# Performance work log

Measured on AMD Instinct MI355X. Metric: run time of the kernel, lower is better.

## Reference

```python
import jax, jax.numpy as jnp
import numpy as np

HIDDEN = 1024
HEADS = 16
HEAD_DIM = HIDDEN // HEADS
SCALE = float(np.sqrt(HEAD_DIM))


def setup_inputs() -> dict:
    key = jax.random.key(0)
    ks = jax.random.split(key, 5)
    x = jax.random.normal(ks[0], (2, 2048, HIDDEN), dtype=jnp.float32)
    # qkv_proj: Linear(hidden, 3*hidden); torch stores weight as [out, in]
    w_qkv = jax.random.normal(ks[1], (3 * HIDDEN, HIDDEN), dtype=jnp.float32) / np.sqrt(HIDDEN)
    b_qkv = jax.random.normal(ks[2], (3 * HIDDEN,), dtype=jnp.float32) * 0.02
    w_out = jax.random.normal(ks[3], (HIDDEN, HIDDEN), dtype=jnp.float32) / np.sqrt(HIDDEN)
    b_out = jax.random.normal(ks[4], (HIDDEN,), dtype=jnp.float32) * 0.02
    return {"x": x, "w_qkv": w_qkv, "b_qkv": b_qkv, "w_out": w_out, "b_out": b_out}


def reference(x, w_qkv, b_qkv, w_out, b_out):
    B, S, H = x.shape
    # fused QKV projection -> [B, S, 3, heads, head_dim]
    qkv = (jnp.einsum('bsh,oh->bso', x, w_qkv) + b_qkv).reshape(B, S, 3, HEADS, HEAD_DIM)
    q, k, v = qkv[:, :, 0], qkv[:, :, 1], qkv[:, :, 2]
    scores = jnp.einsum('bqhd,bkhd->bhqk', q, k) / SCALE
    attn = jax.nn.softmax(scores, axis=-1)  # dropout p=0.0 (eval)
    ctx = jnp.einsum('bhqk,bkhd->bqhd', attn, v).reshape(B, S, H)
    return jnp.einsum('bsh,oh->bso', ctx, w_out) + b_out
```

## Files before the change

### kernel.cpp

```cpp
#include <hip/hip_runtime.h>
#include <math.h>

#define BATCH 2
#define SEQ   2048
#define HIDDEN 1024
#define HEADS 16
#define HD    64
#define QSCALE 0.18033688011112042f

typedef __attribute__((ext_vector_type(8)))  short short8;
typedef __attribute__((ext_vector_type(16))) float f32x16;

__device__ __forceinline__ unsigned short f2bf(float f) {
    unsigned int u = __builtin_bit_cast(unsigned int, f);
    u = (u + 0x7FFFu + ((u >> 16) & 1u)) >> 16;
    return (unsigned short)u;
}
__device__ __forceinline__ float bf2f(unsigned short h) {
    unsigned int u = ((unsigned int)h) << 16;
    return __builtin_bit_cast(float, u);
}
__device__ __forceinline__ unsigned int cvt_pk_bf16(float lo, float hi) {
    unsigned int r;
    asm("v_cvt_pk_bf16_f32 %0, %1, %2" : "=v"(r) : "v"(lo), "v"(hi));
    return r;
}
__device__ __forceinline__ void gl16(const void* g, void* l) {
    __builtin_amdgcn_global_load_lds(
        (const __attribute__((address_space(1))) void*)g,
        (__attribute__((address_space(3))) void*)l,
        16, 0, 0);
}
#define WAIT_VM(N) asm volatile("s_waitcnt vmcnt(" #N ")" ::: "memory")
#define BARRIER()  do { __builtin_amdgcn_s_barrier(); __builtin_amdgcn_sched_barrier(0); } while (0)

__global__ __launch_bounds__(256)
void conv_hi(const float* __restrict__ src, unsigned short* __restrict__ hi)
{
    int idx = blockIdx.x * 256 + threadIdx.x;
    float4 v = ((const float4*)src)[idx];
    ushort4 h4;
    h4.x = f2bf(v.x); h4.y = f2bf(v.y); h4.z = f2bf(v.z); h4.w = f2bf(v.w);
    ((ushort4*)hi)[idx] = h4;
}

__device__ __forceinline__ void gemm_core1(
    const char* Ah, const char* Bh,
    int m0, int n0, char* smem, f32x16 acc[2][2])
{
    const int t    = threadIdx.x;
    const int lane = t & 63;
    const int w    = t >> 6;
    const int wm   = w >> 1, wn = w & 1;
    const int l31  = lane & 31, hh = lane >> 5;

    auto stage = [&](int buf, int kt) {
        #pragma unroll
        for (int i = 0; i < 2; ++i) {
            int r  = i * 64 + (t >> 2);
            int cs = (t & 3) ^ ((r >> 1) & 3);
            gl16(Ah + ((size_t)(m0 + r) * 1024 + kt * 32 + cs * 8) * 2,
                 smem + buf * 16384 + i * 4096 + w * 1024);
            gl16(Bh + ((size_t)(n0 + r) * 1024 + kt * 32 + cs * 8) * 2,
                 smem + buf * 16384 + 8192 + i * 4096 + w * 1024);
        }
    };

    stage(0, 0);
    int cur = 0, nxt = 1;
    for (int kt = 0; kt < 32; ++kt) {
        if (kt + 1 < 32) {
            stage(nxt, kt + 1);
            WAIT_VM(4);
        } else {
            WAIT_VM(0);
        }
        BARRIER();
        const char* Ab = smem + cur * 16384;
        const char* Bb = Ab + 8192;
        #pragma unroll
        for (int ks = 0; ks < 2; ++ks) {
            short8 ah[2], bh[2];
            #pragma unroll
            for (int mt = 0; mt < 2; ++mt) {
                int R  = wm * 64 + mt * 32 + l31;
                int ch = ((ks * 2 + hh) ^ ((R >> 1) & 3)) * 16;
                ah[mt] = *(const short8*)(Ab + R * 64 + ch);
            }
            #pragma unroll
            for (int nt = 0; nt < 2; ++nt) {
                int R  = wn * 64 + nt * 32 + l31;
                int ch = ((ks * 2 + hh) ^ ((R >> 1) & 3)) * 16;
                bh[nt] = *(const short8*)(Bb + R * 64 + ch);
            }
            #pragma unroll
            for (int mt = 0; mt < 2; ++mt)
                #pragma unroll
                for (int nt = 0; nt < 2; ++nt)
                    acc[mt][nt] = __builtin_amdgcn_mfma_f32_32x32x16_bf16(ah[mt], bh[nt], acc[mt][nt], 0, 0, 0);
        }
        cur = nxt;
        nxt = (nxt == 2) ? 0 : nxt + 1;
    }
    __syncthreads();
}

__global__ __launch_bounds__(256, 3)
void qkv_gemm(const unsigned short* __restrict__ xh,
              const unsigned short* __restrict__ wh,
              const float* __restrict__ bias,
              unsigned short* __restrict__ qB, unsigned short* __restrict__ kB,
              unsigned short* __restrict__ vtB)
{
    __shared__ __align__(16) char smem[49152];
    f32x16 acc[2][2] = {{{}, {}}, {{}, {}}};
    const int m0 = blockIdx.x * 128, n0 = blockIdx.y * 128;
    gemm_core1((const char*)xh, (const char*)wh, m0, n0, smem, acc);

    const int t    = threadIdx.x;
    const int lane = t & 63;
    const int w    = t >> 6;
    const int wm   = w >> 1, wn = w & 1;
    const int l31  = lane & 31, hh = lane >> 5;

    const int which = n0 >> 10;
    const float scl = (which == 0) ? QSCALE : 1.0f;

    #pragma unroll
    for (int mt = 0; mt < 2; ++mt)
        #pragma unroll
        for (int nt = 0; nt < 2; ++nt) {
            int nl = wn * 64 + nt * 32 + l31;
            float bb = bias[n0 + nl];
            #pragma unroll
            for (int r = 0; r < 16; ++r) {
                int ml = wm * 64 + mt * 32 + (r & 3) + 8 * (r >> 2) + 4 * hh;
                float val = (acc[mt][nt][r] + bb) * scl;
                *(unsigned short*)(smem + ml * 272 + nl * 2) = f2bf(val);
            }
        }
    __syncthreads();

    const int hbase = (n0 & 1023) >> 6;
    const int b     = m0 >> 11;
    const int s0    = m0 & 2047;

    if (which < 2) {
        unsigned short* pp = which ? kB : qB;
        const int nc   = t & 31;
        const int head = hbase + (nc >> 4);
        const int d0   = (nc & 15) * 4;
        #pragma unroll
        for (int it = 0; it < 16; ++it) {
            int m = it * 8 + (t >> 5);
            ushort4 h4 = *(const ushort4*)(smem + m * 272 + nc * 8);
            size_t idx = (((size_t)(b * HEADS + head)) * SEQ + s0 + m) * HD + d0;
            *(ushort4*)&pp[idx] = h4;
        }
    } else {
        const int nl   = t & 127;
        const int head = hbase + (nl >> 6);
        const int d    = nl & 63;
        #pragma unroll
        for (int it = 0; it < 16; ++it) {
            int mq = it * 2 + (t >> 7);
            ushort4 h4;
            h4.x = *(const unsigned short*)(smem + (mq * 4 + 0) * 272 + nl * 2);
            h4.y = *(const unsigned short*)(smem + (mq * 4 + 1) * 272 + nl * 2);
            h4.z = *(const unsigned short*)(smem + (mq * 4 + 2) * 272 + nl * 2);
            h4.w = *(const unsigned short*)(smem + (mq * 4 + 3) * 272 + nl * 2);
            size_t idx = (((size_t)(b * HEADS + head)) * HD + d) * SEQ + s0 + mq * 4;
            *(ushort4*)&vtB[idx] = h4;
        }
    }
}

__global__ __launch_bounds__(256, 3)
void out_gemm(const unsigned short* __restrict__ cth,
              const unsigned short* __restrict__ bh_,
              const float* __restrict__ bias, float* __restrict__ out)
{
    __shared__ __align__(16) char smem[49152];
    f32x16 acc[2][2] = {{{}, {}}, {{}, {}}};
    const int m0 = blockIdx.x * 128, n0 = blockIdx.y * 128;
    gemm_core1((const char*)cth, (const char*)bh_, m0, n0, smem, acc);

    const int t    = threadIdx.x;
    const int lane = t & 63;
    const int w    = t >> 6;
    const int wm   = w >> 1, wn = w & 1;
    const int l31  = lane & 31, hh = lane >> 5;

    #pragma unroll
    for (int mt = 0; mt < 2; ++mt)
        #pragma unroll
        for (int nt = 0; nt < 2; ++nt) {
            int n = n0 + wn * 64 + nt * 32 + l31;
            float bb = bias[n];
            #pragma unroll
            for (int r = 0; r < 16; ++r) {
                int m = m0 + wm * 64 + mt * 32 + (r & 3) + 8 * (r >> 2) + 4 * hh;
                out[(size_t)m * 1024 + n] = acc[mt][nt][r] + bb;
            }
        }
}

#define NPAIR (SEQ / 64)

__global__ __launch_bounds__(256, 2)
void attn_mfma(const unsigned short* __restrict__ qB, const unsigned short* __restrict__ kB,
               const unsigned short* __restrict__ vtB, unsigned short* __restrict__ ctxb)
{
    __shared__ __align__(16) char smem[65536];
    const int t    = threadIdx.x;
    const int lane = t & 63;
    const int wq   = t >> 6;
    const int l31  = lane & 31;
    const int hh   = lane >> 5;

    const int bid = blockIdx.x;
    const int xcd = bid & 7, j = bid >> 3;
    const int qt  = j & 15;
    const int bhg = xcd + 8 * (j >> 4);
    const int q0  = qt * 128;
    const size_t bh = (size_t)bhg;

    const char* qP = (const char*)(qB + bh * SEQ * HD);
    const char* kP = (const char*)(kB + bh * SEQ * HD);
    const char* vP = (const char*)(vtB + bh * SEQ * HD);

    const int wbase = wq * 1024;

    {
        int rr = t >> 3, cc = t & 7;
        #pragma unroll
        for (int i = 0; i < 4; ++i) {
            int row = i * 32 + rr;
            int ch  = cc ^ (row & 7);
            gl16(qP + (size_t)(q0 + row) * 128 + ch * 16, smem + i * 4096 + wbase);
        }
    }
    auto stagePair = [&](int p) {
        int base = ((p + 1) & 3) * 16384;
        int rr = t >> 3;
        int ch = (t & 7) ^ (rr & 7);
        gl16(kP + (size_t)(p * 64 + rr) * 128 + ch * 16,      smem + base +     0 + wbase);
        gl16(kP + (size_t)(p * 64 + 32 + rr) * 128 + ch * 16, smem + base +  4096 + wbase);
        int rr2 = t >> 2;
        int s4  = (rr2 & 3) ^ ((rr2 >> 2) & 3);
        int ch2 = (t & 3) ^ s4;
        gl16(vP + (size_t)rr2 * (SEQ * 2) + p * 128 +      ch2 * 16, smem + base +  8192 + wbase);
        gl16(vP + (size_t)rr2 * (SEQ * 2) + p * 128 + 64 + ch2 * 16, smem + base + 12288 + wbase);
    };
    stagePair(0);
    stagePair(1);
    WAIT_VM(8);
    BARRIER();

    short8 qf[4];
    {
        int qrow = 32 * wq + l31;
        #pragma unroll
        for (int ks = 0; ks < 4; ++ks) {
            int ch = ((2 * ks + hh) ^ (qrow & 7)) * 16;
            qf[ks] = *(const short8*)(smem + qrow * 128 + ch);
        }
    }
    asm volatile("s_waitcnt lgkmcnt(0)" ::: "memory");
    __builtin_amdgcn_sched_barrier(0);

    f32x16 acc0 = {}, acc1 = {};
    float lsum = 0.0f;

    for (int i = 0; i < NPAIR; ++i) {
        if (i + 2 < NPAIR) { stagePair(i + 2); WAIT_VM(8); }
        else if (i + 1 < NPAIR) { WAIT_VM(4); }
        else { WAIT_VM(0); }
        BARRIER();

        const char* Pb = smem + ((i + 1) & 3) * 16384;

        f32x16 sa = {}, sb = {};
        __builtin_amdgcn_s_setprio(1);
        #pragma unroll
        for (int ks = 0; ks < 4; ++ks) {
            int ch = ((2 * ks + hh) ^ (l31 & 7)) * 16;
            short8 ka = *(const short8*)(Pb +        l31 * 128 + ch);
            short8 kb = *(const short8*)(Pb + 4096 + l31 * 128 + ch);
            sa = __builtin_amdgcn_mfma_f32_32x32x16_bf16(ka, qf[ks], sa, 0, 0, 0);
            sb = __builtin_amdgcn_mfma_f32_32x32x16_bf16(kb, qf[ks], sb, 0, 0, 0);
        }
        __builtin_amdgcn_s_setprio(0);

        unsigned int pa_[8], pb_[8];
        float ps0 = 0.f, ps1 = 0.f, ps2 = 0.f, ps3 = 0.f;
        #pragma unroll
        for (int w = 0; w < 8; ++w) {
            float e0 = __builtin_amdgcn_exp2f(sa[2 * w]);
            float e1 = __builtin_amdgcn_exp2f(sa[2 * w + 1]);
            ps0 += e0; ps1 += e1;
            pa_[w] = cvt_pk_bf16(e0, e1);
            float f0 = __builtin_amdgcn_exp2f(sb[2 * w]);
            float f1 = __builtin_amdgcn_exp2f(sb[2 * w + 1]);
            ps2 += f0; ps3 += f1;
            pb_[w] = cvt_pk_bf16(f0, f1);
        }
        lsum += (ps0 + ps1) + (ps2 + ps3);

        const char* Va = Pb + 8192;
        const char* Vb = Pb + 12288;
        __builtin_amdgcn_s_setprio(1);
        #pragma unroll
        for (int ks = 0; ks < 2; ++ks) {
            unsigned int a0 = pa_[4*ks],     a2 = pa_[4*ks + 2];
            unsigned int a1 = pa_[4*ks + 1], a3 = pa_[4*ks + 3];
            asm volatile("v_permlane32_swap_b32 %0, %1" : "+v"(a0), "+v"(a2));
            asm volatile("v_permlane32_swap_b32 %0, %1" : "+v"(a1), "+v"(a3));
            unsigned int b0 = pb_[4*ks],     b2 = pb_[4*ks + 2];
            unsigned int b1 = pb_[4*ks + 1], b3 = pb_[4*ks + 3];
            asm volatile("v_permlane32_swap_b32 %0, %1" : "+v"(b0), "+v"(b2));
            asm volatile("v_permlane32_swap_b32 %0, %1" : "+v"(b1), "+v"(b3));
            short8 pA = __builtin_bit_cast(short8, make_uint4(a0, a1, a2, a3));
            short8 pB = __builtin_bit_cast(short8, make_uint4(b0, b1, b2, b3));
            #pragma unroll
            for (int mt = 0; mt < 2; ++mt) {
                int rrow = 32 * mt + l31;
                int s4   = (rrow & 3) ^ ((rrow >> 2) & 3);
                int ch   = ((2 * ks + hh) ^ s4) * 16;
                short8 va = *(const short8*)(Va + rrow * 64 + ch);
                short8 vb = *(const short8*)(Vb + rrow * 64 + ch);
                if (mt == 0) {
                    acc0 = __builtin_amdgcn_mfma_f32_32x32x16_bf16(va, pA, acc0, 0, 0, 0);
                    acc0 = __builtin_amdgcn_mfma_f32_32x32x16_bf16(vb, pB, acc0, 0, 0, 0);
                } else {
                    acc1 = __builtin_amdgcn_mfma_f32_32x32x16_bf16(va, pA, acc1, 0, 0, 0);
                    acc1 = __builtin_amdgcn_mfma_f32_32x32x16_bf16(vb, pB, acc1, 0, 0, 0);
                }
            }
        }
        __builtin_amdgcn_s_setprio(0);
    }

    lsum += __shfl_xor(lsum, 32, 64);
    __syncthreads();
    float inv = 1.0f / lsum;
    {
        int q = 32 * wq + l31;
        #pragma unroll
        for (int mt = 0; mt < 2; ++mt) {
            #pragma unroll
            for (int m2 = 0; m2 < 4; ++m2) {
                ushort4 h4;
                if (mt == 0) {
                    h4.x = f2bf(acc0[4*m2+0] * inv); h4.y = f2bf(acc0[4*m2+1] * inv);
                    h4.z = f2bf(acc0[4*m2+2] * inv); h4.w = f2bf(acc0[4*m2+3] * inv);
                } else {
                    h4.x = f2bf(acc1[4*m2+0] * inv); h4.y = f2bf(acc1[4*m2+1] * inv);
                    h4.z = f2bf(acc1[4*m2+2] * inv); h4.w = f2bf(acc1[4*m2+3] * inv);
                }
                int d0 = 4 * hh + 8 * m2 + 32 * mt;
                int c  = (d0 >> 3) ^ (q & 7);
                *(ushort4*)(smem + q * 128 + c * 16 + (d0 & 7) * 2) = h4;
            }
        }
    }
    __syncthreads();
    {
        #pragma unroll
        for (int it = 0; it < 4; ++it) {
            int slot = it * 256 + t;
            int row  = slot >> 3;
            int p    = slot & 7;
            uint4 v4 = *(const uint4*)(smem + row * 128 + ((p ^ (row & 7)) * 16));
            *(uint4*)&ctxb[((size_t)(bhg >> 4) * SEQ + q0 + row) * HIDDEN
                           + (bhg & 15) * HD + p * 8] = v4;
        }
    }
}

extern "C" void kernel_launch(void* const* d_in, const int* in_sizes, int n_in,
                              void* d_out, int out_size, void* d_ws, size_t ws_size,
                              hipStream_t stream)
{
    const float* x     = (const float*)d_in[0];
    const float* w_qkv = (const float*)d_in[1];
    const float* b_qkv = (const float*)d_in[2];
    const float* w_out = (const float*)d_in[3];
    const float* b_out = (const float*)d_in[4];
    float* out = (float*)d_out;

    const size_t PH = (size_t)BATCH * HEADS * SEQ * HD;
    unsigned short* ws = (unsigned short*)d_ws;
    unsigned short* qB  = ws;
    unsigned short* kB  = ws + PH;
    unsigned short* vtB = ws + 2 * PH;
    unsigned short* wqh = ws + 3 * PH;
    unsigned short* woh = wqh + 3 * PH / 4;
    unsigned short* cth = woh + PH / 4;
    unsigned short* xh  = (unsigned short*)d_out;

    conv_hi<<<4096, 256, 0, stream>>>(x, xh);
    conv_hi<<<3072, 256, 0, stream>>>(w_qkv, wqh);
    conv_hi<<<1024, 256, 0, stream>>>(w_out, woh);
    qkv_gemm<<<dim3(32, 24), 256, 0, stream>>>(xh, wqh, b_qkv, qB, kB, vtB);
    attn_mfma<<<512, 256, 0, stream>>>(qB, kB, vtB, cth);
    out_gemm<<<dim3(32, 8), 256, 0, stream>>>(cth, woh, b_out, out);
}
```

Before: 114.0 us.

## Software-pipeline QK^T one tile ahead in attention and merge conversion launches

The attention loop now computes the QK^T scores for the next K/V pair before doing the exp and PV work for the current pair. This lets MFMA score work overlap with the softmax exponentials and the V matmul. The vmcnt waits are loosened to match. Separately, the three fp32-to-bf16 conversion launches are merged into one kernel that picks its source from the block index, saving launch overhead. The trade-off is more live registers from the extra score accumulators, which could lower occupancy, and more complex wait-count logic that has to stay correct.

```diff
diff --git a/kernel.cpp b/kernel.cpp
--- a/kernel.cpp
+++ b/kernel.cpp
@@ -16,10 +16,6 @@
     u = (u + 0x7FFFu + ((u >> 16) & 1u)) >> 16;
     return (unsigned short)u;
 }
-__device__ __forceinline__ float bf2f(unsigned short h) {
-    unsigned int u = ((unsigned int)h) << 16;
-    return __builtin_bit_cast(float, u);
-}
 __device__ __forceinline__ unsigned int cvt_pk_bf16(float lo, float hi) {
     unsigned int r;
     asm("v_cvt_pk_bf16_f32 %0, %1, %2" : "=v"(r) : "v"(lo), "v"(hi));
@@ -35,13 +31,22 @@
 #define BARRIER()  do { __builtin_amdgcn_s_barrier(); __builtin_amdgcn_sched_barrier(0); } while (0)
 
 __global__ __launch_bounds__(256)
-void conv_hi(const float* __restrict__ src, unsigned short* __restrict__ hi)
-{
-    int idx = blockIdx.x * 256 + threadIdx.x;
+void conv_all(const float* __restrict__ x,  unsigned short* __restrict__ xh,
+              const float* __restrict__ wq, unsigned short* __restrict__ wqh,
+              const float* __restrict__ wo, unsigned short* __restrict__ woh)
+{
+    int b = blockIdx.x;
+    const float* src;
+    unsigned short* dst;
+    int base;
+    if (b < 4096)      { src = x;  dst = xh;  base = b; }
+    else if (b < 7168) { src = wq; dst = wqh; base = b - 4096; }
+    else               { src = wo; dst = woh; base = b - 7168; }
+    int idx = base * 256 + threadIdx.x;
     float4 v = ((const float4*)src)[idx];
     ushort4 h4;
     h4.x = f2bf(v.x); h4.y = f2bf(v.y); h4.z = f2bf(v.z); h4.w = f2bf(v.w);
-    ((ushort4*)hi)[idx] = h4;
+    ((ushort4*)dst)[idx] = h4;
 }
 
 __device__ __forceinline__ void gemm_core1(
@@ -268,19 +273,12 @@
     }
     asm volatile("s_waitcnt lgkmcnt(0)" ::: "memory");
     __builtin_amdgcn_sched_barrier(0);
-
-    f32x16 acc0 = {}, acc1 = {};
-    float lsum = 0.0f;
-
-    for (int i = 0; i < NPAIR; ++i) {
-        if (i + 2 < NPAIR) { stagePair(i + 2); WAIT_VM(8); }
-        else if (i + 1 < NPAIR) { WAIT_VM(4); }
-        else { WAIT_VM(0); }
-        BARRIER();
-
-        const char* Pb = smem + ((i + 1) & 3) * 16384;
-
-        f32x16 sa = {}, sb = {};
+    WAIT_VM(4);
+    BARRIER();
+
+    f32x16 sa = {}, sb = {};
+    {
+        const char* Pb = smem + 16384;
         __builtin_amdgcn_s_setprio(1);
         #pragma unroll
         for (int ks = 0; ks < 4; ++ks) {
@@ -291,6 +289,30 @@
             sb = __builtin_amdgcn_mfma_f32_32x32x16_bf16(kb, qf[ks], sb, 0, 0, 0);
         }
         __builtin_amdgcn_s_setprio(0);
+    }
+
+    f32x16 acc0 = {}, acc1 = {};
+    float lsum = 0.0f;
+
+    for (int i = 0; i < NPAIR; ++i) {
+        if (i + 2 < NPAIR) { stagePair(i + 2); WAIT_VM(4); }
+        else if (i + 1 < NPAIR) { WAIT_VM(0); }
+        BARRIER();
+
+        f32x16 na = {}, nb = {};
+        if (i + 1 < NPAIR) {
+            const char* Pn = smem + ((i + 2) & 3) * 16384;
+            __builtin_amdgcn_s_setprio(1);
+            #pragma unroll
+            for (int ks = 0; ks < 4; ++ks) {
+                int ch = ((2 * ks + hh) ^ (l31 & 7)) * 16;
+                short8 ka = *(const short8*)(Pn +        l31 * 128 + ch);
+                short8 kb = *(const short8*)(Pn + 4096 + l31 * 128 + ch);
+                na = __builtin_amdgcn_mfma_f32_32x32x16_bf16(ka, qf[ks], na, 0, 0, 0);
+                nb = __builtin_amdgcn_mfma_f32_32x32x16_bf16(kb, qf[ks], nb, 0, 0, 0);
+            }
+            __builtin_amdgcn_s_setprio(0);
+        }
 
         unsigned int pa_[8], pb_[8];
         float ps0 = 0.f, ps1 = 0.f, ps2 = 0.f, ps3 = 0.f;
@@ -307,6 +329,7 @@
         }
         lsum += (ps0 + ps1) + (ps2 + ps3);
 
+        const char* Pb = smem + ((i + 1) & 3) * 16384;
         const char* Va = Pb + 8192;
         const char* Vb = Pb + 12288;
         __builtin_amdgcn_s_setprio(1);
@@ -339,6 +362,8 @@
             }
         }
         __builtin_amdgcn_s_setprio(0);
+
+        sa = na; sb = nb;
     }
 
     lsum += __shfl_xor(lsum, 32, 64);
@@ -399,9 +424,7 @@
     unsigned short* cth = woh + PH / 4;
     unsigned short* xh  = (unsigned short*)d_out;
 
-    conv_hi<<<4096, 256, 0, stream>>>(x, xh);
-    conv_hi<<<3072, 256, 0, stream>>>(w_qkv, wqh);
-    conv_hi<<<1024, 256, 0, stream>>>(w_out, woh);
+    conv_all<<<8192, 256, 0, stream>>>(x, xh, w_qkv, wqh, w_out, woh);
     qkv_gemm<<<dim3(32, 24), 256, 0, stream>>>(xh, wqh, b_qkv, qB, kB, vtB);
     attn_mfma<<<512, 256, 0, stream>>>(qB, kB, vtB, cth);
     out_gemm<<<dim3(32, 8), 256, 0, stream>>>(cth, woh, b_out, out);
```

Result: faster. 110.6 us (-3.0%).
